# Performance work log

Measured on AMD Instinct MI355X. Metric: run time of the kernel, lower is better.

## Reference

```python
import jax, jax.numpy as jnp
import numpy as np

B, S, E = 2, 2048, 1024
H, D = 16, 64  # num_head, num_hidden
EPS = 1e-5

def setup_inputs() -> dict:
    key = jax.random.key(0)
    ks = jax.random.split(key, 12)
    sc_e = 1.0 / np.sqrt(E)
    sc_hd = 1.0 / np.sqrt(H * D)
    return {
        "q": jax.random.normal(ks[0], (B, S, E), jnp.float32),
        "k": jax.random.normal(ks[1], (B, S, E), jnp.float32),
        "v": jax.random.normal(ks[2], (B, S, E), jnp.float32),
        "Wq": jax.random.normal(ks[3], (E, H * D), jnp.float32) * sc_e,
        "bq": jnp.zeros((H * D,), jnp.float32),
        "Wk": jax.random.normal(ks[4], (E, H * D), jnp.float32) * sc_e,
        "bk": jnp.zeros((H * D,), jnp.float32),
        "Wv": jax.random.normal(ks[5], (E, H * D), jnp.float32) * sc_e,
        "bv": jnp.zeros((H * D,), jnp.float32),
        "Wo": jax.random.normal(ks[6], (H * D, E), jnp.float32) * sc_hd,
        "bo": jnp.zeros((E,), jnp.float32),
        "gamma": jnp.ones((E,), jnp.float32),
        "beta": jnp.zeros((E,), jnp.float32),
    }

def reference(q, k, v, Wq, bq, Wk, bk, Wv, bv, Wo, bo, gamma, beta):
    # QKV projections -> [B, H, S, D]
    q_ = (q @ Wq + bq).reshape(B, S, H, D).transpose(0, 2, 1, 3)
    k_ = (k @ Wk + bk).reshape(B, S, H, D).transpose(0, 2, 1, 3)
    v_ = (v @ Wv + bv).reshape(B, S, H, D).transpose(0, 2, 1, 3)
    # scaled dot-product attention scores [B, H, Sq, Sk]
    qk = jnp.einsum('bhid,bhjd->bhij', q_, k_) / np.sqrt(D)
    attn = jax.nn.softmax(qk, axis=-1)
    # weighted values -> [B, Sq, H, D] -> [B, Sq, H*D]
    outs = jnp.einsum('bhij,bhjd->bihd', attn, v_).reshape(B, S, H * D)
    outs = outs @ Wo + bo
    # residual + LayerNorm
    x = outs + q
    mu = jnp.mean(x, axis=-1, keepdims=True)
    var = jnp.var(x, axis=-1, keepdims=True)
    y = (x - mu) * jax.lax.rsqrt(var + EPS) * gamma + beta
    return (y, attn)
```

## Files before the change

### kernel.cpp

```cpp
#include <hip/hip_runtime.h>

typedef unsigned short u16;
typedef __attribute__((ext_vector_type(8))) short bf16x8;
typedef __attribute__((ext_vector_type(4))) float f32x4;
typedef __attribute__((ext_vector_type(4))) unsigned short u16x4;

static __device__ __forceinline__ u16 f2bf(float f) {
  unsigned int u = __builtin_bit_cast(unsigned int, f);
  u += 0x7fffu + ((u >> 16) & 1u);
  return (u16)(u >> 16);
}

static __device__ __forceinline__ void load_lds16(const void* g, void* l) {
  __builtin_amdgcn_global_load_lds(
      (const __attribute__((address_space(1))) void*)g,
      (__attribute__((address_space(3))) void*)l,
      16, 0, 0);
}

__global__ __launch_bounds__(256) void to_bf16_3(const float* __restrict__ a,
                                                 const float* __restrict__ b,
                                                 const float* __restrict__ c,
                                                 u16* __restrict__ oa,
                                                 u16* __restrict__ ob,
                                                 u16* __restrict__ oc, int n4) {
  const int z = blockIdx.y;
  const float* in = (z == 0) ? a : (z == 1) ? b : c;
  u16* out = (z == 0) ? oa : (z == 1) ? ob : oc;
  int i = blockIdx.x * 256 + threadIdx.x;
  if (i < n4) {
    float4 f = ((const float4*)in)[i];
    u16x4 u;
    u[0] = f2bf(f.x); u[1] = f2bf(f.y); u[2] = f2bf(f.z); u[3] = f2bf(f.w);
    ((u16x4*)out)[i] = u;
  }
}

__global__ __launch_bounds__(256) void transpose_bf16(const float* __restrict__ W,
                                                      u16* __restrict__ WT) {
  __shared__ float t[32][33];
  const int tx = threadIdx.x, ty = threadIdx.y;
  const int bx = blockIdx.x * 32, by = blockIdx.y * 32;
#pragma unroll
  for (int r = ty; r < 32; r += 8) t[r][tx] = W[(size_t)(by + r) * 1024 + bx + tx];
  __syncthreads();
#pragma unroll
  for (int r = ty; r < 32; r += 8) WT[(size_t)(bx + r) * 1024 + by + tx] = f2bf(t[tx][r]);
}

__device__ __forceinline__ void gemm_core(const u16* __restrict__ A,
                                          const u16* __restrict__ BT,
                                          int m0, int n0,
                                          u16* As, u16* Bs, f32x4 acc[4][4]) {
  const int tid = threadIdx.x;
  const int w = tid >> 6, l = tid & 63;
  const int lr = l & 15, lg = l >> 4;
  const int wm = w >> 1, wn = w & 1;

  const int p0 = tid * 16, p1 = p0 + 4096;
  const char* gA0 = (const char*)A + (size_t)(m0 + (p0 >> 6)) * 2048 + (p0 & 63);
  const char* gA1 = (const char*)A + (size_t)(m0 + (p1 >> 6)) * 2048 + (p1 & 63);
  const char* gB0 = (const char*)BT + (size_t)(n0 + (p0 >> 6)) * 2048 + (p0 & 63);
  const char* gB1 = (const char*)BT + (size_t)(n0 + (p1 >> 6)) * 2048 + (p1 & 63);
  char* lA0 = (char*)As + w * 1024;
  char* lA1 = (char*)As + 4096 + w * 1024;
  char* lB0 = (char*)Bs + w * 1024;
  char* lB1 = (char*)Bs + 4096 + w * 1024;

  for (int kt = 0; kt < 32; ++kt) {
    const int kb = kt * 64;
    load_lds16(gA0 + kb, lA0);
    load_lds16(gA1 + kb, lA1);
    load_lds16(gB0 + kb, lB0);
    load_lds16(gB1 + kb, lB1);
    __syncthreads();
    bf16x8 av[4], bv[4];
#pragma unroll
    for (int f = 0; f < 4; ++f) {
      av[f] = *(const bf16x8*)(As + (wm * 64 + f * 16 + lr) * 32 + lg * 8);
      bv[f] = *(const bf16x8*)(Bs + (wn * 64 + f * 16 + lr) * 32 + lg * 8);
    }
#pragma unroll
    for (int fm = 0; fm < 4; ++fm)
#pragma unroll
      for (int fn = 0; fn < 4; ++fn)
        acc[fm][fn] = __builtin_amdgcn_mfma_f32_16x16x32_bf16(av[fm], bv[fn],
                                                              acc[fm][fn], 0, 0, 0);
    __syncthreads();
  }
}

__global__ __launch_bounds__(256) void qkv_gemm(
    const u16* __restrict__ qb, const u16* __restrict__ kbm, const u16* __restrict__ vbm,
    const u16* __restrict__ WqT, const u16* __restrict__ WkT, const u16* __restrict__ WvT,
    const float* __restrict__ bq, const float* __restrict__ bk, const float* __restrict__ bv,
    u16* __restrict__ Qb, u16* __restrict__ Kb, u16* __restrict__ Vt) {
  __shared__ u16 As[4096], Bs[4096];
  const int z = blockIdx.z;
  const u16* A = (z == 0) ? qb : (z == 1) ? kbm : vbm;
  const u16* BT = (z == 0) ? WqT : (z == 1) ? WkT : WvT;
  const float* bias = (z == 0) ? bq : (z == 1) ? bk : bv;
  const int m0 = blockIdx.y * 128, n0 = blockIdx.x * 128;

  f32x4 acc[4][4];
#pragma unroll
  for (int i = 0; i < 4; ++i)
#pragma unroll
    for (int j = 0; j < 4; ++j) acc[i][j] = (f32x4){0.f, 0.f, 0.f, 0.f};

  gemm_core(A, BT, m0, n0, As, Bs, acc);

  const int tid = threadIdx.x;
  const int w = tid >> 6, l = tid & 63, lr = l & 15, lg = l >> 4;
  const int wm = w >> 1, wn = w & 1;
#pragma unroll
  for (int fm = 0; fm < 4; ++fm)
#pragma unroll
    for (int fn = 0; fn < 4; ++fn)
#pragma unroll
      for (int r = 0; r < 4; ++r) {
        const int m = m0 + wm * 64 + fm * 16 + lg * 4 + r;
        const int n = n0 + wn * 64 + fn * 16 + lr;
        const float val = acc[fm][fn][r] + bias[n];
        const int b = m >> 11, s = m & 2047, hh = n >> 6, d = n & 63;
        const u16 u = f2bf(val);
        if (z == 2)
          Vt[(((size_t)b * 16 + hh) * 64 + d) * 2048 + s] = u;
        else if (z == 0)
          Qb[(((size_t)b * 16 + hh) * 2048 + s) * 64 + d] = u;
        else
          Kb[(((size_t)b * 16 + hh) * 2048 + s) * 64 + d] = u;
      }
}

__global__ __launch_bounds__(256) void o_gemm(
    const u16* __restrict__ Ao, const u16* __restrict__ WoT,
    const float* __restrict__ bo, const float* __restrict__ resid,
    float* __restrict__ x) {
  __shared__ u16 As[4096], Bs[4096];
  const int m0 = blockIdx.y * 128, n0 = blockIdx.x * 128;
  f32x4 acc[4][4];
#pragma unroll
  for (int i = 0; i < 4; ++i)
#pragma unroll
    for (int j = 0; j < 4; ++j) acc[i][j] = (f32x4){0.f, 0.f, 0.f, 0.f};

  gemm_core(Ao, WoT, m0, n0, As, Bs, acc);

  const int tid = threadIdx.x;
  const int w = tid >> 6, l = tid & 63, lr = l & 15, lg = l >> 4;
  const int wm = w >> 1, wn = w & 1;
#pragma unroll
  for (int fm = 0; fm < 4; ++fm)
#pragma unroll
    for (int fn = 0; fn < 4; ++fn)
#pragma unroll
      for (int r = 0; r < 4; ++r) {
        const int m = m0 + wm * 64 + fm * 16 + lg * 4 + r;
        const int n = n0 + wn * 64 + fn * 16 + lr;
        const size_t idx = (size_t)m * 1024 + n;
        x[idx] = acc[fm][fn][r] + bo[n] + resid[idx];
      }
}

__global__ __launch_bounds__(256, 4) void denom_kernel(
    const u16* __restrict__ Qb, const u16* __restrict__ Kb,
    float* __restrict__ Ld) {
  __shared__ u16 Kbuf[2][4096];
  const int tid = threadIdx.x;
  const int w = tid >> 6, l = tid & 63, lr = l & 15, lg = l >> 4;

  int flat = blockIdx.x;
  flat = (flat & 7) * 64 + (flat >> 3);
  const int it = flat & 15, bh = flat >> 4;
  const int i0 = it * 128;

  const char* KhB = (const char*)(Kb + (size_t)bh * 2048 * 64);
  const u16* Q0 = Qb + ((size_t)bh * 2048 + i0 + w * 32 + lr) * 64;
  const bf16x8 q00 = *(const bf16x8*)(Q0 + lg * 8);
  const bf16x8 q01 = *(const bf16x8*)(Q0 + 32 + lg * 8);
  const bf16x8 q10 = *(const bf16x8*)(Q0 + 16 * 64 + lg * 8);
  const bf16x8 q11 = *(const bf16x8*)(Q0 + 16 * 64 + 32 + lg * 8);

  const int srow = l >> 3;
  const int soff = ((l & 7) ^ srow) << 4;
  const int rsw = (lr & 7) << 4;

#define STAGE_K(bb, j0)                                                      \
  load_lds16(KhB + (size_t)((j0) + w * 8 + srow) * 128 + soff,               \
             (char*)Kbuf[bb] + w * 1024);                                    \
  load_lds16(KhB + (size_t)((j0) + 32 + w * 8 + srow) * 128 + soff,          \
             (char*)Kbuf[bb] + w * 1024 + 4096);

  f32x4 ls0 = (f32x4){0.f, 0.f, 0.f, 0.f}, ls1 = ls0;
  STAGE_K(0, 0);
  __syncthreads();
  for (int jt = 0; jt < 32; ++jt) {
    const int bb = jt & 1;
    if (jt < 31) { STAGE_K(bb ^ 1, (jt + 1) * 64); }
    const char* kb = (const char*)Kbuf[bb];
#pragma unroll
    for (int t = 0; t < 4; ++t) {
      const bf16x8 k0 = *(const bf16x8*)(kb + (t * 16 + lr) * 128 + ((lg * 16) ^ rsw));
      const bf16x8 k1 = *(const bf16x8*)(kb + (t * 16 + lr) * 128 + ((64 + lg * 16) ^ rsw));
      f32x4 c0 = (f32x4){0.f, 0.f, 0.f, 0.f}, c1 = c0;
      c0 = __builtin_amdgcn_mfma_f32_16x16x32_bf16(k0, q00, c0, 0, 0, 0);
      c0 = __builtin_amdgcn_mfma_f32_16x16x32_bf16(k1, q01, c0, 0, 0, 0);
      c1 = __builtin_amdgcn_mfma_f32_16x16x32_bf16(k0, q10, c1, 0, 0, 0);
      c1 = __builtin_amdgcn_mfma_f32_16x16x32_bf16(k1, q11, c1, 0, 0, 0);
      ls0[0] += __expf(c0[0] * 0.125f);
      ls0[1] += __expf(c0[1] * 0.125f);
      ls0[2] += __expf(c0[2] * 0.125f);
      ls0[3] += __expf(c0[3] * 0.125f);
      ls1[0] += __expf(c1[0] * 0.125f);
      ls1[1] += __expf(c1[1] * 0.125f);
      ls1[2] += __expf(c1[2] * 0.125f);
      ls1[3] += __expf(c1[3] * 0.125f);
    }
    __syncthreads();
  }
#undef STAGE_K
  float s0 = ls0[0] + ls0[1] + ls0[2] + ls0[3];
  s0 += __shfl_xor(s0, 16);
  s0 += __shfl_xor(s0, 32);
  float s1 = ls1[0] + ls1[1] + ls1[2] + ls1[3];
  s1 += __shfl_xor(s1, 16);
  s1 += __shfl_xor(s1, 32);
  if (l < 16) {
    Ld[(size_t)bh * 2048 + i0 + w * 32 + l] = s0;
    Ld[(size_t)bh * 2048 + i0 + w * 32 + 16 + l] = s1;
  }
}

__global__ __launch_bounds__(256, 4) void attn3_kernel(
    const u16* __restrict__ Qb, const u16* __restrict__ Kb,
    const u16* __restrict__ Vt, const float* __restrict__ Ld,
    float* __restrict__ attnG, u16* __restrict__ outattn) {
  __shared__ u16 Kbuf[2][4096];
  __shared__ u16 Vbuf[2][4096];
  __shared__ u16 Pbuf[4][1024];
  const int tid = threadIdx.x;
  const int w = tid >> 6, l = tid & 63, lr = l & 15, lg = l >> 4;

  int flat = (blockIdx.z * 16 + blockIdx.y) * 32 + blockIdx.x;
  flat = (flat & 7) * 128 + (flat >> 3);
  const int qt = flat & 31, h = (flat >> 5) & 15, b = flat >> 9;
  const int bh = b * 16 + h;
  const int i0 = qt * 64 + w * 16;

  const char* KhB = (const char*)(Kb + (size_t)bh * 2048 * 64);
  const char* VhB = (const char*)(Vt + (size_t)bh * 64 * 2048);
  const u16* Qrow = Qb + ((size_t)bh * 2048 + i0 + lr) * 64;
  const bf16x8 bq0 = *(const bf16x8*)(Qrow + lg * 8);
  const bf16x8 bq1 = *(const bf16x8*)(Qrow + 32 + lg * 8);
  const float inv = 1.f / Ld[(size_t)bh * 2048 + i0 + lr];

  const int srow = l >> 3;
  const int soff = ((l & 7) ^ srow) << 4;
  const int rsw = (lr & 7) << 4;

#define STAGE_K(bb, j0)                                                      \
  load_lds16(KhB + (size_t)((j0) + w * 8 + srow) * 128 + soff,               \
             (char*)Kbuf[bb] + w * 1024);                                    \
  load_lds16(KhB + (size_t)((j0) + 32 + w * 8 + srow) * 128 + soff,          \
             (char*)Kbuf[bb] + w * 1024 + 4096);
#define STAGE_V(bb, j0)                                                      \
  load_lds16(VhB + (size_t)(w * 8 + srow) * 4096 + (size_t)(j0) * 2 + soff,  \
             (char*)Vbuf[bb] + w * 1024);                                    \
  load_lds16(VhB + (size_t)(32 + w * 8 + srow) * 4096 + (size_t)(j0) * 2 +   \
                 soff,                                                       \
             (char*)Vbuf[bb] + w * 1024 + 4096);

  float* const awb = attnG + ((size_t)bh * 2048 + i0 + (l >> 4)) * 2048 + (l & 15) * 4;
  char* const Pw = (char*)Pbuf[w];
  f32x4 o0 = (f32x4){0.f, 0.f, 0.f, 0.f}, o1 = o0, o2 = o0, o3 = o0;

  STAGE_K(0, 0);
  STAGE_V(0, 0);
  __syncthreads();
  for (int jt = 0; jt < 32; ++jt) {
    const int bb = jt & 1;
    if (jt < 31) {
      STAGE_K(bb ^ 1, (jt + 1) * 64);
      STAGE_V(bb ^ 1, (jt + 1) * 64);
    }
    const char* kb = (const char*)Kbuf[bb];
    const char* vb = (const char*)Vbuf[bb];
    const int j0 = jt * 64;
#pragma unroll
    for (int t = 0; t < 4; ++t) {
      const bf16x8 k0 = *(const bf16x8*)(kb + (t * 16 + lr) * 128 + ((lg * 16) ^ rsw));
      const bf16x8 k1 = *(const bf16x8*)(kb + (t * 16 + lr) * 128 + ((64 + lg * 16) ^ rsw));
      f32x4 c = (f32x4){0.f, 0.f, 0.f, 0.f};
      c = __builtin_amdgcn_mfma_f32_16x16x32_bf16(k0, bq0, c, 0, 0, 0);
      c = __builtin_amdgcn_mfma_f32_16x16x32_bf16(k1, bq1, c, 0, 0, 0);
      u16x4 pu;
      pu[0] = f2bf(__expf(c[0] * 0.125f) * inv);
      pu[1] = f2bf(__expf(c[1] * 0.125f) * inv);
      pu[2] = f2bf(__expf(c[2] * 0.125f) * inv);
      pu[3] = f2bf(__expf(c[3] * 0.125f) * inv);
      *(u16x4*)(Pw + lr * 128 + ((t * 32 + lg * 8) ^ rsw)) = pu;
    }
#pragma unroll
    for (int rq = 0; rq < 4; ++rq) {
      const int row = rq * 4 + (l >> 4);
      const u16x4 pb = *(const u16x4*)(Pw + row * 128 +
                                       (((l & 15) * 8) ^ ((row & 7) << 4)));
      f32x4 pf;
      pf[0] = __builtin_bit_cast(float, (unsigned)(unsigned short)pb[0] << 16);
      pf[1] = __builtin_bit_cast(float, (unsigned)(unsigned short)pb[1] << 16);
      pf[2] = __builtin_bit_cast(float, (unsigned)(unsigned short)pb[2] << 16);
      pf[3] = __builtin_bit_cast(float, (unsigned)(unsigned short)pb[3] << 16);
      __builtin_nontemporal_store(pf, (f32x4*)(awb + (size_t)(rq * 4) * 2048 + j0));
    }
#pragma unroll
    for (int half = 0; half < 2; ++half) {
      const int jjb = half * 64;
      const bf16x8 pa = *(const bf16x8*)(Pw + lr * 128 + ((jjb + lg * 16) ^ rsw));
      const bf16x8 v0 = *(const bf16x8*)(vb + (0 * 16 + lr) * 128 + ((jjb + lg * 16) ^ rsw));
      const bf16x8 v1 = *(const bf16x8*)(vb + (1 * 16 + lr) * 128 + ((jjb + lg * 16) ^ rsw));
      const bf16x8 v2 = *(const bf16x8*)(vb + (2 * 16 + lr) * 128 + ((jjb + lg * 16) ^ rsw));
      const bf16x8 v3 = *(const bf16x8*)(vb + (3 * 16 + lr) * 128 + ((jjb + lg * 16) ^ rsw));
      o0 = __builtin_amdgcn_mfma_f32_16x16x32_bf16(pa, v0, o0, 0, 0, 0);
      o1 = __builtin_amdgcn_mfma_f32_16x16x32_bf16(pa, v1, o1, 0, 0, 0);
      o2 = __builtin_amdgcn_mfma_f32_16x16x32_bf16(pa, v2, o2, 0, 0, 0);
      o3 = __builtin_amdgcn_mfma_f32_16x16x32_bf16(pa, v3, o3, 0, 0, 0);
    }
    asm volatile("s_waitcnt vmcnt(4)" ::: "memory");
    __builtin_amdgcn_sched_barrier(0);
    __builtin_amdgcn_s_barrier();
  }
#undef STAGE_K
#undef STAGE_V

#pragma unroll
  for (int r = 0; r < 4; ++r) {
    u16* orow = outattn + ((size_t)b * 2048 + i0 + lg * 4 + r) * 1024 + h * 64 + lr;
    orow[0]  = f2bf(o0[r]);
    orow[16] = f2bf(o1[r]);
    orow[32] = f2bf(o2[r]);
    orow[48] = f2bf(o3[r]);
  }
}

__global__ __launch_bounds__(256) void ln_kernel(const float* __restrict__ x,
                                                 const float* __restrict__ gamma,
                                                 const float* __restrict__ beta,
                                                 float* __restrict__ y) {
  const int row = blockIdx.x, t = threadIdx.x;
  const float4 xv = *(const float4*)(x + (size_t)row * 1024 + t * 4);
  float s = xv.x + xv.y + xv.z + xv.w;
  float q2 = xv.x * xv.x + xv.y * xv.y + xv.z * xv.z + xv.w * xv.w;
#pragma unroll
  for (int off = 32; off >= 1; off >>= 1) {
    s += __shfl_xor(s, off);
    q2 += __shfl_xor(q2, off);
  }
  __shared__ float ps[4], pq[4];
  const int w = t >> 6, l = t & 63;
  if (l == 0) { ps[w] = s; pq[w] = q2; }
  __syncthreads();
  s = ps[0] + ps[1] + ps[2] + ps[3];
  q2 = pq[0] + pq[1] + pq[2] + pq[3];
  const float mu = s * (1.f / 1024.f);
  const float var = q2 * (1.f / 1024.f) - mu * mu;
  const float rs = rsqrtf(var + 1e-5f);
  const float4 g = *(const float4*)(gamma + t * 4);
  const float4 bb = *(const float4*)(beta + t * 4);
  float4 o;
  o.x = (xv.x - mu) * rs * g.x + bb.x;
  o.y = (xv.y - mu) * rs * g.y + bb.y;
  o.z = (xv.z - mu) * rs * g.z + bb.z;
  o.w = (xv.w - mu) * rs * g.w + bb.w;
  *(float4*)(y + (size_t)row * 1024 + t * 4) = o;
}

extern "C" void kernel_launch(void* const* d_in, const int* in_sizes, int n_in,
                              void* d_out, int out_size, void* d_ws, size_t ws_size,
                              hipStream_t stream) {
  (void)in_sizes; (void)n_in; (void)out_size; (void)ws_size;
  const float* q = (const float*)d_in[0];
  const float* k = (const float*)d_in[1];
  const float* v = (const float*)d_in[2];
  const float* Wq = (const float*)d_in[3];
  const float* bq = (const float*)d_in[4];
  const float* Wk = (const float*)d_in[5];
  const float* bk = (const float*)d_in[6];
  const float* Wv = (const float*)d_in[7];
  const float* bv = (const float*)d_in[8];
  const float* Wo = (const float*)d_in[9];
  const float* bo = (const float*)d_in[10];
  const float* gamma = (const float*)d_in[11];
  const float* beta = (const float*)d_in[12];

  char* ws = (char*)d_ws;
  const size_t MB = 1ull << 20;
  u16* WqT = (u16*)(ws + 0 * MB);
  u16* WkT = (u16*)(ws + 2 * MB);
  u16* WvT = (u16*)(ws + 4 * MB);
  u16* WoT = (u16*)(ws + 6 * MB);
  u16* qb  = (u16*)(ws + 8 * MB);
  float* Ld = (float*)(ws + 10 * MB);
  u16* kb  = (u16*)(ws + 16 * MB);
  u16* vb  = (u16*)(ws + 24 * MB);
  u16* Qb  = (u16*)(ws + 32 * MB);
  u16* Kb  = (u16*)(ws + 40 * MB);
  u16* Vt  = (u16*)(ws + 48 * MB);
  u16* oa  = (u16*)(ws + 56 * MB);
  float* x = (float*)(ws + 64 * MB);

  float* y = (float*)d_out;
  float* attnG = y + 4194304;

  to_bf16_3<<<dim3(4096, 3), 256, 0, stream>>>(q, k, v, qb, kb, vb, 1048576);
  transpose_bf16<<<dim3(32, 32), dim3(32, 8), 0, stream>>>(Wq, WqT);
  transpose_bf16<<<dim3(32, 32), dim3(32, 8), 0, stream>>>(Wk, WkT);
  transpose_bf16<<<dim3(32, 32), dim3(32, 8), 0, stream>>>(Wv, WvT);
  transpose_bf16<<<dim3(32, 32), dim3(32, 8), 0, stream>>>(Wo, WoT);
  qkv_gemm<<<dim3(8, 32, 3), 256, 0, stream>>>(qb, kb, vb, WqT, WkT, WvT,
                                               bq, bk, bv, Qb, Kb, Vt);
  denom_kernel<<<512, 256, 0, stream>>>(Qb, Kb, Ld);
  attn3_kernel<<<dim3(32, 16, 2), 256, 0, stream>>>(Qb, Kb, Vt, Ld, attnG, oa);
  o_gemm<<<dim3(8, 32), 256, 0, stream>>>(oa, WoT, bo, q, x);
  ln_kernel<<<4096, 256, 0, stream>>>(x, gamma, beta, y);
}
```

Measured before the change: 262.0 us.

## Double-buffer GEMM LDS staging, merge weight transposes, relax attention wait count

The shared GEMM core now double-buffers its LDS tiles, issuing the next k-tile's global-to-LDS loads before the MFMAs on the current tile so load latency overlaps compute. This doubles LDS use per block and puts a full vmcnt wait and barrier at the end of each iteration. The four weight-transpose launches are merged into one launch with a z-dimension, which cuts launch overhead. The attention kernel's wait count is raised from 4 to 16 so more loads stay in flight; this is only correct if the outstanding-load ordering still guarantees the needed tile has arrived.

```diff
diff --git a/kernel.cpp b/kernel.cpp
--- a/kernel.cpp
+++ b/kernel.cpp
@@ -36,10 +36,16 @@
   }
 }
 
-__global__ __launch_bounds__(256) void transpose_bf16(const float* __restrict__ W,
-                                                      u16* __restrict__ WT) {
+__global__ __launch_bounds__(256) void transpose_bf16_4(
+    const float* __restrict__ Wq, const float* __restrict__ Wk,
+    const float* __restrict__ Wv, const float* __restrict__ Wo,
+    u16* __restrict__ WqT, u16* __restrict__ WkT,
+    u16* __restrict__ WvT, u16* __restrict__ WoT) {
+  const int z = blockIdx.z;
+  const float* W = (z == 0) ? Wq : (z == 1) ? Wk : (z == 2) ? Wv : Wo;
+  u16* WT = (z == 0) ? WqT : (z == 1) ? WkT : (z == 2) ? WvT : WoT;
   __shared__ float t[32][33];
-  const int tx = threadIdx.x, ty = threadIdx.y;
+  const int tx = threadIdx.x & 31, ty = threadIdx.x >> 5;
   const int bx = blockIdx.x * 32, by = blockIdx.y * 32;
 #pragma unroll
   for (int r = ty; r < 32; r += 8) t[r][tx] = W[(size_t)(by + r) * 1024 + bx + tx];
@@ -62,23 +68,25 @@
   const char* gA1 = (const char*)A + (size_t)(m0 + (p1 >> 6)) * 2048 + (p1 & 63);
   const char* gB0 = (const char*)BT + (size_t)(n0 + (p0 >> 6)) * 2048 + (p0 & 63);
   const char* gB1 = (const char*)BT + (size_t)(n0 + (p1 >> 6)) * 2048 + (p1 & 63);
-  char* lA0 = (char*)As + w * 1024;
-  char* lA1 = (char*)As + 4096 + w * 1024;
-  char* lB0 = (char*)Bs + w * 1024;
-  char* lB1 = (char*)Bs + 4096 + w * 1024;
-
+
+#define GCSTAGE(bb, kb)                                                      \
+  load_lds16(gA0 + (kb), (char*)As + (bb) * 8192 + w * 1024);                \
+  load_lds16(gA1 + (kb), (char*)As + (bb) * 8192 + 4096 + w * 1024);         \
+  load_lds16(gB0 + (kb), (char*)Bs + (bb) * 8192 + w * 1024);                \
+  load_lds16(gB1 + (kb), (char*)Bs + (bb) * 8192 + 4096 + w * 1024);
+
+  GCSTAGE(0, 0);
+  __syncthreads();
   for (int kt = 0; kt < 32; ++kt) {
-    const int kb = kt * 64;
-    load_lds16(gA0 + kb, lA0);
-    load_lds16(gA1 + kb, lA1);
-    load_lds16(gB0 + kb, lB0);
-    load_lds16(gB1 + kb, lB1);
-    __syncthreads();
+    const int bb = kt & 1;
+    if (kt < 31) { GCSTAGE(bb ^ 1, (kt + 1) * 64); }
+    const u16* as = As + bb * 4096;
+    const u16* bs = Bs + bb * 4096;
     bf16x8 av[4], bv[4];
 #pragma unroll
     for (int f = 0; f < 4; ++f) {
-      av[f] = *(const bf16x8*)(As + (wm * 64 + f * 16 + lr) * 32 + lg * 8);
-      bv[f] = *(const bf16x8*)(Bs + (wn * 64 + f * 16 + lr) * 32 + lg * 8);
+      av[f] = *(const bf16x8*)(as + (wm * 64 + f * 16 + lr) * 32 + lg * 8);
+      bv[f] = *(const bf16x8*)(bs + (wn * 64 + f * 16 + lr) * 32 + lg * 8);
     }
 #pragma unroll
     for (int fm = 0; fm < 4; ++fm)
@@ -86,8 +94,11 @@
       for (int fn = 0; fn < 4; ++fn)
         acc[fm][fn] = __builtin_amdgcn_mfma_f32_16x16x32_bf16(av[fm], bv[fn],
                                                               acc[fm][fn], 0, 0, 0);
-    __syncthreads();
-  }
+    asm volatile("s_waitcnt vmcnt(0)" ::: "memory");
+    __builtin_amdgcn_sched_barrier(0);
+    __builtin_amdgcn_s_barrier();
+  }
+#undef GCSTAGE
 }
 
 __global__ __launch_bounds__(256) void qkv_gemm(
@@ -95,7 +106,7 @@
     const u16* __restrict__ WqT, const u16* __restrict__ WkT, const u16* __restrict__ WvT,
     const float* __restrict__ bq, const float* __restrict__ bk, const float* __restrict__ bv,
     u16* __restrict__ Qb, u16* __restrict__ Kb, u16* __restrict__ Vt) {
-  __shared__ u16 As[4096], Bs[4096];
+  __shared__ u16 As[2 * 4096], Bs[2 * 4096];
   const int z = blockIdx.z;
   const u16* A = (z == 0) ? qb : (z == 1) ? kbm : vbm;
   const u16* BT = (z == 0) ? WqT : (z == 1) ? WkT : WvT;
@@ -137,7 +148,7 @@
     const u16* __restrict__ Ao, const u16* __restrict__ WoT,
     const float* __restrict__ bo, const float* __restrict__ resid,
     float* __restrict__ x) {
-  __shared__ u16 As[4096], Bs[4096];
+  __shared__ u16 As[2 * 4096], Bs[2 * 4096];
   const int m0 = blockIdx.y * 128, n0 = blockIdx.x * 128;
   f32x4 acc[4][4];
 #pragma unroll
@@ -326,7 +337,7 @@
       o2 = __builtin_amdgcn_mfma_f32_16x16x32_bf16(pa, v2, o2, 0, 0, 0);
       o3 = __builtin_amdgcn_mfma_f32_16x16x32_bf16(pa, v3, o3, 0, 0, 0);
     }
-    asm volatile("s_waitcnt vmcnt(4)" ::: "memory");
+    asm volatile("s_waitcnt vmcnt(16)" ::: "memory");
     __builtin_amdgcn_sched_barrier(0);
     __builtin_amdgcn_s_barrier();
   }
@@ -413,10 +424,8 @@
   float* attnG = y + 4194304;
 
   to_bf16_3<<<dim3(4096, 3), 256, 0, stream>>>(q, k, v, qb, kb, vb, 1048576);
-  transpose_bf16<<<dim3(32, 32), dim3(32, 8), 0, stream>>>(Wq, WqT);
-  transpose_bf16<<<dim3(32, 32), dim3(32, 8), 0, stream>>>(Wk, WkT);
-  transpose_bf16<<<dim3(32, 32), dim3(32, 8), 0, stream>>>(Wv, WvT);
-  transpose_bf16<<<dim3(32, 32), dim3(32, 8), 0, stream>>>(Wo, WoT);
+  transpose_bf16_4<<<dim3(32, 32, 4), 256, 0, stream>>>(Wq, Wk, Wv, Wo,
+                                                        WqT, WkT, WvT, WoT);
   qkv_gemm<<<dim3(8, 32, 3), 256, 0, stream>>>(qb, kb, vb, WqT, WkT, WvT,
                                                bq, bk, bv, Qb, Kb, Vt);
   denom_kernel<<<512, 256, 0, stream>>>(Qb, Kb, Ld);
```

After: 264.5 us. No clear change (+1.0%).
